# Optimization experiments

Hardware: AMD Instinct MI355X
Metric: run time of the kernel (lower is better)

## Reference

```python
import jax, jax.numpy as jnp
import numpy as np

N = 20000       # nodes
E = 640000      # random edges (self-loops appended -> E + N total)
G = 64          # graphs in batch
F_IN = 114
H1 = 3          # heads in layer 1
D2 = 128        # output_dim of layer 2
NEG = 0.2       # GATConv leaky_relu negative slope


def setup_inputs() -> dict:
    key = jax.random.key(0)
    ks = jax.random.split(key, 20)
    x = jax.random.normal(ks[0], (N, F_IN), jnp.float32)
    src = jax.random.randint(ks[1], (E,), 0, N, jnp.int32)
    dst = jax.random.randint(ks[2], (E,), 0, N, jnp.int32)
    loop = jnp.arange(N, dtype=jnp.int32)  # PyG add_self_loops=True
    edge_index = jnp.stack([jnp.concatenate([src, loop]),
                            jnp.concatenate([dst, loop])])
    batch = (jnp.arange(N) * G // N).astype(jnp.int32)  # every graph non-empty

    def lin(k, i, o):
        return jax.random.normal(k, (i, o), jnp.float32) * (1.0 / np.sqrt(i))

    return {
        "x": x, "edge_index": edge_index, "batch": batch,
        # GATConv 1: 114 -> 114 per head, 3 heads, concat
        "W1": lin(ks[3], F_IN, H1 * F_IN),
        "a_src1": jax.random.normal(ks[4], (H1, F_IN), jnp.float32) * 0.1,
        "a_dst1": jax.random.normal(ks[5], (H1, F_IN), jnp.float32) * 0.1,
        "b1": jnp.zeros((H1 * F_IN,), jnp.float32),
        # GATConv 2: 342 -> 128, 1 head
        "W2": lin(ks[6], H1 * F_IN, D2),
        "a_src2": jax.random.normal(ks[7], (1, D2), jnp.float32) * 0.1,
        "a_dst2": jax.random.normal(ks[8], (1, D2), jnp.float32) * 0.1,
        "b2": jnp.zeros((D2,), jnp.float32),
        # MLP head
        "Wg": lin(ks[9], D2, 64),  "bg": jnp.zeros((64,), jnp.float32),
        "Wf1": lin(ks[10], 64, 32), "bf1": jnp.zeros((32,), jnp.float32),
        "Wf2": lin(ks[11], 32, 16), "bf2": jnp.zeros((16,), jnp.float32),
        "Wo": lin(ks[12], 16, 1),   "bo": jnp.zeros((1,), jnp.float32),
    }


def gat_conv(x, edge_index, W, a_src, a_dst, b, heads, dim):
    """PyG GATConv (self-loops already in edge_index, eval mode)."""
    n = x.shape[0]
    h = (x @ W).reshape(n, heads, dim)             # [N,H,D]
    src, dst = edge_index[0], edge_index[1]
    alpha_s = jnp.sum(h * a_src, axis=-1)          # [N,H]
    alpha_d = jnp.sum(h * a_dst, axis=-1)          # [N,H]
    e = jax.nn.leaky_relu(alpha_s[src] + alpha_d[dst], NEG)  # [E,H]
    # segment softmax over destination nodes
    m = jax.ops.segment_max(e, dst, num_segments=n)
    ex = jnp.exp(e - m[dst])
    s = jax.ops.segment_sum(ex, dst, num_segments=n)
    alpha = ex / s[dst]                            # [E,H]
    out = jax.ops.segment_sum(h[src] * alpha[..., None], dst, num_segments=n)
    return out.reshape(n, heads * dim) + b


def reference(x, edge_index, batch, W1, a_src1, a_dst1, b1,
              W2, a_src2, a_dst2, b2, Wg, bg, Wf1, bf1, Wf2, bf2, Wo, bo):
    h = jax.nn.elu(gat_conv(x, edge_index, W1, a_src1, a_dst1, b1, H1, F_IN))
    h = jax.nn.relu(gat_conv(h, edge_index, W2, a_src2, a_dst2, b2, 1, D2))
    g = jax.ops.segment_max(h, batch, num_segments=G)   # global max pool [G,128]
    g = jax.nn.relu(g @ Wg + bg)
    g = jax.nn.relu(g @ Wf1 + bf1)
    g = jax.nn.relu(g @ Wf2 + bf2)
    return g @ Wo + bo                                  # [G,1]
```

## Files before the change

kernel.cpp:

```cpp
#include <hip/hip_runtime.h>

#define NN 20000
#define EE 660000
#define GG 64
#define FIN 114
#define H1 3
#define F1 342
#define D2 128
#define NEG 0.2f
#define H1AS 352

__device__ inline unsigned fenc(float f) {
    unsigned u = __float_as_uint(f);
    return (u & 0x80000000u) ? ~u : (u | 0x80000000u);
}
__device__ inline float fdec(unsigned u) {
    return (u & 0x80000000u) ? __uint_as_float(u & 0x7FFFFFFFu) : __uint_as_float(~u);
}
__device__ inline float lrelu(float x) { return x > 0.f ? x : NEG * x; }

__global__ void k_wa(const float* __restrict__ W1, const float* __restrict__ aS,
                     const float* __restrict__ aD, float* __restrict__ was,
                     float* __restrict__ wad) {
    int tid = blockIdx.x * 256 + threadIdx.x;
    if (tid >= 2 * FIN * H1) return;
    int which = tid >= FIN * H1;
    int i = which ? tid - FIN * H1 : tid;
    int k = i / H1, h = i % H1;
    const float* a = which ? aD : aS;
    float s = 0.f;
    for (int d = 0; d < FIN; d++) s += W1[k * F1 + h * FIN + d] * a[h * FIN + d];
    (which ? wad : was)[i] = s;
}

__global__ void k_prep1(const float* __restrict__ W1, float* __restrict__ W1P) {
    int tid = blockIdx.x * 256 + threadIdx.x;
    if (tid >= H1 * 128 * 128) return;
    int h = tid / (128 * 128);
    int rem = tid & (128 * 128 - 1);
    int k = rem >> 7, c = rem & 127;
    W1P[tid] = (c < FIN && k < FIN) ? W1[k * F1 + h * FIN + c] : 0.f;
}

__global__ __launch_bounds__(256) void k_alpha1x(const float* __restrict__ x,
                                                 const float* __restrict__ was,
                                                 const float* __restrict__ wad,
                                                 float* __restrict__ as1,
                                                 float* __restrict__ ad1) {
    int n = blockIdx.x * 4 + (threadIdx.x >> 6);
    int l = threadIdx.x & 63;
    if (n >= NN) return;
    float x0 = x[n * FIN + l];
    float x1 = (l < FIN - 64) ? x[n * FIN + 64 + l] : 0.f;
    float s[H1], d[H1];
#pragma unroll
    for (int h = 0; h < H1; h++) {
        float w0s = was[l * H1 + h], w0d = wad[l * H1 + h];
        float w1s = (l < FIN - 64) ? was[(64 + l) * H1 + h] : 0.f;
        float w1d = (l < FIN - 64) ? wad[(64 + l) * H1 + h] : 0.f;
        s[h] = x0 * w0s + x1 * w1s;
        d[h] = x0 * w0d + x1 * w1d;
    }
#pragma unroll
    for (int o = 32; o > 0; o >>= 1) {
#pragma unroll
        for (int h = 0; h < H1; h++) {
            s[h] += __shfl_down(s[h], o);
            d[h] += __shfl_down(d[h], o);
        }
    }
    if (l == 0) {
#pragma unroll
        for (int h = 0; h < H1; h++) {
            as1[n * H1 + h] = s[h];
            ad1[n * H1 + h] = d[h];
        }
    }
}

__global__ void k_count(const int* __restrict__ dst, int* __restrict__ cnt) {
    int e = blockIdx.x * 256 + threadIdx.x;
    if (e < EE) atomicAdd(&cnt[dst[e]], 1);
}

__global__ __launch_bounds__(1024) void k_scan(const int* __restrict__ cnt,
                                               int* __restrict__ off) {
    __shared__ int part[1024];
    int t = threadIdx.x;
    const int CH = 20;
    int loc[CH];
    int s = 0;
    int base = t * CH;
    for (int i = 0; i < CH; i++) {
        int idx = base + i;
        int v = (idx < NN) ? cnt[idx] : 0;
        loc[i] = s;
        s += v;
    }
    part[t] = s;
    __syncthreads();
    for (int d = 1; d < 1024; d <<= 1) {
        int v = (t >= d) ? part[t - d] : 0;
        __syncthreads();
        part[t] += v;
        __syncthreads();
    }
    int pre = (t == 0) ? 0 : part[t - 1];
    for (int i = 0; i < CH; i++) {
        int idx = base + i;
        if (idx < NN) off[idx] = pre + loc[i];
    }
    if (t == 1023) off[NN] = part[1023];
}

__global__ void k_scatter(const int* __restrict__ src, const int* __restrict__ dst,
                          const int* __restrict__ off, int* __restrict__ cur,
                          int* __restrict__ csr_src) {
    int e = blockIdx.x * 256 + threadIdx.x;
    if (e < EE) {
        int d = dst[e];
        int pos = off[d] + atomicAdd(&cur[d], 1);
        csr_src[pos] = src[e];
    }
}

__global__ __launch_bounds__(128) void k_aggx(const float* __restrict__ x,
                                              const float* __restrict__ as1,
                                              const float* __restrict__ ad1,
                                              const int* __restrict__ off,
                                              const int* __restrict__ csr_src,
                                              float* __restrict__ xaggP) {
    int n = blockIdx.x, t = threadIdx.x;
    int e0 = off[n], e1 = off[n + 1];
    float adv0 = ad1[n * H1 + 0], adv1 = ad1[n * H1 + 1], adv2 = ad1[n * H1 + 2];
    __shared__ int ssrc[64];
    __shared__ float sw[64][H1];
    __shared__ float red[64][H1];
    float acc0 = 0.f, acc1 = 0.f, acc2 = 0.f;
    float ps0 = 0.f, ps1 = 0.f, ps2 = 0.f;
    for (int base = e0; base < e1; base += 64) {
        int c = min(64, e1 - base);
        __syncthreads();
        if (t < c) {
            int s = csr_src[base + t];
            ssrc[t] = s;
            float w0 = __expf(lrelu(as1[s * H1 + 0] + adv0));
            float w1 = __expf(lrelu(as1[s * H1 + 1] + adv1));
            float w2 = __expf(lrelu(as1[s * H1 + 2] + adv2));
            sw[t][0] = w0; sw[t][1] = w1; sw[t][2] = w2;
            ps0 += w0; ps1 += w1; ps2 += w2;
        }
        __syncthreads();
        if (t < FIN) {
            for (int j = 0; j < c; j++) {
                float xv = x[ssrc[j] * FIN + t];
                acc0 += xv * sw[j][0];
                acc1 += xv * sw[j][1];
                acc2 += xv * sw[j][2];
            }
        }
    }
    __syncthreads();
    if (t < 64) { red[t][0] = ps0; red[t][1] = ps1; red[t][2] = ps2; }
    __syncthreads();
    for (int sr = 32; sr > 0; sr >>= 1) {
        if (t < sr) {
            red[t][0] += red[t + sr][0];
            red[t][1] += red[t + sr][1];
            red[t][2] += red[t + sr][2];
        }
        __syncthreads();
    }
    float i0 = 1.f / red[0][0], i1 = 1.f / red[0][1], i2 = 1.f / red[0][2];
    float v0 = (t < FIN) ? acc0 * i0 : 0.f;
    float v1 = (t < FIN) ? acc1 * i1 : 0.f;
    float v2 = (t < FIN) ? acc2 * i2 : 0.f;
    xaggP[(size_t)0 * NN * 128 + n * 128 + t] = v0;
    xaggP[(size_t)1 * NN * 128 + n * 128 + t] = v1;
    xaggP[(size_t)2 * NN * 128 + n * 128 + t] = v2;
}

__global__ __launch_bounds__(256) void k_gemm1t(const float* __restrict__ xaggP,
                                                const float* __restrict__ W1P,
                                                const float* __restrict__ b1,
                                                float* __restrict__ h1aP) {
    int h = blockIdx.y;
    int rb = blockIdx.x * 64;
    int t = threadIdx.x;
    int tr = t >> 4, tc = t & 15;
    __shared__ float As[64][36];
    __shared__ float Bs[32][132];
    const float* Ap = xaggP + (size_t)h * NN * 128;
    const float* Bp = W1P + (size_t)h * 128 * 128;
    const float4 zf4 = make_float4(0.f, 0.f, 0.f, 0.f);

    int ar0 = t >> 3, ak0 = t & 7;
    int ar1 = 32 + ar0;
    int bk[4], bn[4];
#pragma unroll
    for (int q = 0; q < 4; q++) { int idd = t + q * 256; bk[q] = idd >> 5; bn[q] = idd & 31; }

    float4 aR[2], bR[4];
    {
        int g0 = rb + ar0, g1 = rb + ar1;
        aR[0] = (g0 < NN) ? *(const float4*)(Ap + (size_t)g0 * 128 + ak0 * 4) : zf4;
        aR[1] = (g1 < NN) ? *(const float4*)(Ap + (size_t)g1 * 128 + ak0 * 4) : zf4;
#pragma unroll
        for (int q = 0; q < 4; q++)
            bR[q] = *(const float4*)(Bp + (size_t)bk[q] * 128 + bn[q] * 4);
    }
    float acc[4][8] = {};
    for (int tile = 0; tile < 4; tile++) {
        if (tile) __syncthreads();
        *(float4*)(&As[ar0][ak0 * 4]) = aR[0];
        *(float4*)(&As[ar1][ak0 * 4]) = aR[1];
#pragma unroll
        for (int q = 0; q < 4; q++) *(float4*)(&Bs[bk[q]][bn[q] * 4]) = bR[q];
        __syncthreads();
        if (tile < 3) {
            int k0 = (tile + 1) * 32;
            int g0 = rb + ar0, g1 = rb + ar1;
            aR[0] = (g0 < NN) ? *(const float4*)(Ap + (size_t)g0 * 128 + k0 + ak0 * 4) : zf4;
            aR[1] = (g1 < NN) ? *(const float4*)(Ap + (size_t)g1 * 128 + k0 + ak0 * 4) : zf4;
#pragma unroll
            for (int q = 0; q < 4; q++)
                bR[q] = *(const float4*)(Bp + (size_t)(k0 + bk[q]) * 128 + bn[q] * 4);
        }
#pragma unroll
        for (int kc = 0; kc < 32; kc += 4) {
            float a4[4][4];
#pragma unroll
            for (int r = 0; r < 4; r++)
                *(float4*)a4[r] = *(const float4*)(&As[tr * 4 + r][kc]);
#pragma unroll
            for (int kk = 0; kk < 4; kk++) {
                float4 b0 = *(const float4*)(&Bs[kc + kk][tc * 4]);
                float4 b1v = *(const float4*)(&Bs[kc + kk][64 + tc * 4]);
#pragma unroll
                for (int r = 0; r < 4; r++) {
                    float av = a4[r][kk];
                    acc[r][0] += av * b0.x;  acc[r][1] += av * b0.y;
                    acc[r][2] += av * b0.z;  acc[r][3] += av * b0.w;
                    acc[r][4] += av * b1v.x; acc[r][5] += av * b1v.y;
                    acc[r][6] += av * b1v.z; acc[r][7] += av * b1v.w;
                }
            }
        }
    }
    int hb = h * FIN;
#pragma unroll
    for (int r = 0; r < 4; r++) {
        int row = rb + tr * 4 + r;
        if (row >= NN) continue;
        float* orow = h1aP + (size_t)row * H1AS + hb;
#pragma unroll
        for (int j = 0; j < 8; j++) {
            int c = (j < 4) ? (tc * 4 + j) : (64 + tc * 4 + (j - 4));
            if (c < FIN) {
                float v = acc[r][j] + b1[hb + c];
                orow[c] = v > 0.f ? v : expm1f(v);
            } else if (h == 2 && c < 124) {
                orow[c] = 0.f;
            }
        }
    }
}

__global__ __launch_bounds__(256) void k_gemm2t(const float* __restrict__ h1aP,
                                                const float* __restrict__ W2,
                                                float* __restrict__ h2) {
    int mt = blockIdx.x >> 1, nb = (blockIdx.x & 1) * 64;
    int rb = mt * 64;
    int t = threadIdx.x;
    int tr = t >> 4, tc = t & 15;
    __shared__ float As[64][36];
    __shared__ float Bs[32][68];
    const float4 zf4 = make_float4(0.f, 0.f, 0.f, 0.f);
    int ar0 = t >> 3, ak0 = t & 7;
    int ar1 = 32 + ar0;
    int bk0 = t >> 4, bn0 = t & 15;
    int bk1 = 16 + bk0;
    float4 aR[2], bR[2];
    {
        int g0 = rb + ar0, g1 = rb + ar1;
        aR[0] = (g0 < NN) ? *(const float4*)(h1aP + (size_t)g0 * H1AS + ak0 * 4) : zf4;
        aR[1] = (g1 < NN) ? *(const float4*)(h1aP + (size_t)g1 * H1AS + ak0 * 4) : zf4;
        bR[0] = *(const float4*)(W2 + (size_t)bk0 * D2 + nb + bn0 * 4);
        bR[1] = *(const float4*)(W2 + (size_t)bk1 * D2 + nb + bn0 * 4);
    }
    float acc[4][4] = {};
    for (int tile = 0; tile < 11; tile++) {
        if (tile) __syncthreads();
        *(float4*)(&As[ar0][ak0 * 4]) = aR[0];
        *(float4*)(&As[ar1][ak0 * 4]) = aR[1];
        *(float4*)(&Bs[bk0][bn0 * 4]) = bR[0];
        *(float4*)(&Bs[bk1][bn0 * 4]) = bR[1];
        __syncthreads();
        if (tile < 10) {
            int k0 = (tile + 1) * 32;
            int g0 = rb + ar0, g1 = rb + ar1;
            aR[0] = (g0 < NN) ? *(const float4*)(h1aP + (size_t)g0 * H1AS + k0 + ak0 * 4) : zf4;
            aR[1] = (g1 < NN) ? *(const float4*)(h1aP + (size_t)g1 * H1AS + k0 + ak0 * 4) : zf4;
            bR[0] = (k0 + bk0 < F1) ? *(const float4*)(W2 + (size_t)(k0 + bk0) * D2 + nb + bn0 * 4) : zf4;
            bR[1] = (k0 + bk1 < F1) ? *(const float4*)(W2 + (size_t)(k0 + bk1) * D2 + nb + bn0 * 4) : zf4;
        }
#pragma unroll
        for (int kc = 0; kc < 32; kc += 4) {
            float a4[4][4];
#pragma unroll
            for (int r = 0; r < 4; r++)
                *(float4*)a4[r] = *(const float4*)(&As[tr * 4 + r][kc]);
#pragma unroll
            for (int kk = 0; kk < 4; kk++) {
                float4 b0 = *(const float4*)(&Bs[kc + kk][tc * 4]);
#pragma unroll
                for (int r = 0; r < 4; r++) {
                    float av = a4[r][kk];
                    acc[r][0] += av * b0.x; acc[r][1] += av * b0.y;
                    acc[r][2] += av * b0.z; acc[r][3] += av * b0.w;
                }
            }
        }
    }
#pragma unroll
    for (int r = 0; r < 4; r++) {
        int row = rb + tr * 4 + r;
        if (row < NN)
            *(float4*)(&h2[(size_t)row * D2 + nb + tc * 4]) =
                make_float4(acc[r][0], acc[r][1], acc[r][2], acc[r][3]);
    }
}

__global__ __launch_bounds__(256) void k_alpha2(const float* __restrict__ h2,
                                                const float* __restrict__ aS,
                                                const float* __restrict__ aD,
                                                float* __restrict__ as2,
                                                float* __restrict__ ad2) {
    int n = blockIdx.x * 4 + (threadIdx.x >> 6);
    int l = threadIdx.x & 63;
    if (n >= NN) return;
    float v0 = h2[(size_t)n * D2 + l], v1 = h2[(size_t)n * D2 + 64 + l];
    float ps = v0 * aS[l] + v1 * aS[64 + l];
    float pd = v0 * aD[l] + v1 * aD[64 + l];
    for (int o = 32; o > 0; o >>= 1) {
        ps += __shfl_down(ps, o);
        pd += __shfl_down(pd, o);
    }
    if (l == 0) {
        as2[n] = ps;
        ad2[n] = pd;
    }
}

__global__ __launch_bounds__(128) void k_agg2f(const float* __restrict__ h2,
                                               const float* __restrict__ as2,
                                               const float* __restrict__ ad2,
                                               const int* __restrict__ off,
                                               const int* __restrict__ csr_src,
                                               const float* __restrict__ b2,
                                               unsigned* __restrict__ poolbuf) {
    int n = blockIdx.x, t = threadIdx.x;
    int e0 = off[n], e1 = off[n + 1];
    float adv = ad2[n];
    __shared__ int ssrc[64];
    __shared__ float sw[64];
    __shared__ float red[64];
    float acc = 0.f, ps = 0.f;
    for (int base = e0; base < e1; base += 64) {
        int c = min(64, e1 - base);
        __syncthreads();
        if (t < c) {
            int s = csr_src[base + t];
            ssrc[t] = s;
            float w = __expf(lrelu(as2[s] + adv));
            sw[t] = w;
            ps += w;
        }
        __syncthreads();
        for (int j = 0; j < c; j++) acc += h2[(size_t)ssrc[j] * D2 + t] * sw[j];
    }
    __syncthreads();
    if (t < 64) red[t] = ps;
    __syncthreads();
    for (int sr = 32; sr > 0; sr >>= 1) {
        if (t < sr) red[t] += red[t + sr];
        __syncthreads();
    }
    float v = fmaxf(acc / red[0] + b2[t], 0.f);
    int g = (int)(((long long)n * GG) / NN);
    atomicMax(&poolbuf[g * D2 + t], fenc(v));
}

__global__ __launch_bounds__(128) void k_mlp(const unsigned* __restrict__ poolbuf,
                                             const float* __restrict__ Wg,
                                             const float* __restrict__ bg,
                                             const float* __restrict__ Wf1,
                                             const float* __restrict__ bf1,
                                             const float* __restrict__ Wf2,
                                             const float* __restrict__ bf2,
                                             const float* __restrict__ Wo,
                                             const float* __restrict__ bo,
                                             float* __restrict__ out) {
    int g = blockIdx.x;
    int t = threadIdx.x;
    __shared__ float pool[D2];
    __shared__ float a1[64];
    __shared__ float a2[32];
    __shared__ float a3[16];
    pool[t] = fdec(poolbuf[g * D2 + t]);
    __syncthreads();
    if (t < 64) {
        float acc = bg[t];
        for (int k = 0; k < D2; k++) acc += pool[k] * Wg[k * 64 + t];
        a1[t] = fmaxf(acc, 0.f);
    }
    __syncthreads();
    if (t < 32) {
        float acc = bf1[t];
        for (int k = 0; k < 64; k++) acc += a1[k] * Wf1[k * 32 + t];
        a2[t] = fmaxf(acc, 0.f);
    }
    __syncthreads();
    if (t < 16) {
        float acc = bf2[t];
        for (int k = 0; k < 32; k++) acc += a2[k] * Wf2[k * 16 + t];
        a3[t] = fmaxf(acc, 0.f);
    }
    __syncthreads();
    if (t == 0) {
        float acc = bo[0];
        for (int k = 0; k < 16; k++) acc += a3[k] * Wo[k];
        out[g] = acc;
    }
}

extern "C" void kernel_launch(void* const* d_in, const int* in_sizes, int n_in,
                              void* d_out, int out_size, void* d_ws, size_t ws_size,
                              hipStream_t stream) {
    const float* x = (const float*)d_in[0];
    const int* ei = (const int*)d_in[1];
    const float* W1 = (const float*)d_in[3];
    const float* aS1 = (const float*)d_in[4];
    const float* aD1 = (const float*)d_in[5];
    const float* b1 = (const float*)d_in[6];
    const float* W2 = (const float*)d_in[7];
    const float* aS2 = (const float*)d_in[8];
    const float* aD2 = (const float*)d_in[9];
    const float* b2 = (const float*)d_in[10];
    const float* Wg = (const float*)d_in[11];
    const float* bg = (const float*)d_in[12];
    const float* Wf1 = (const float*)d_in[13];
    const float* bf1 = (const float*)d_in[14];
    const float* Wf2 = (const float*)d_in[15];
    const float* bf2 = (const float*)d_in[16];
    const float* Wo = (const float*)d_in[17];
    const float* bo = (const float*)d_in[18];
    float* out = (float*)d_out;

    const int* src = ei;
    const int* dst = ei + EE;

    char* ws = (char*)d_ws;
    size_t o = 0;
    auto alloc = [&](size_t bytes) -> char* {
        char* p = ws + o;
        o += (bytes + 255) & ~(size_t)255;
        return p;
    };
    float* was = (float*)alloc((size_t)FIN * H1 * 4);
    float* wad = (float*)alloc((size_t)FIN * H1 * 4);
    float* W1P = (float*)alloc((size_t)H1 * 128 * 128 * 4);
    float* as1 = (float*)alloc((size_t)NN * H1 * 4);
    float* ad1 = (float*)alloc((size_t)NN * H1 * 4);
    int* cnt = (int*)alloc((size_t)NN * 4);
    int* off = (int*)alloc((size_t)(NN + 1) * 4);
    int* cur = (int*)alloc((size_t)NN * 4);
    int* csr_src = (int*)alloc((size_t)EE * 4);
    float* xaggP = (float*)alloc((size_t)H1 * NN * 128 * 4);
    float* h1aP = (float*)alloc((size_t)NN * H1AS * 4);
    float* h2 = (float*)alloc((size_t)NN * D2 * 4);
    float* as2 = (float*)alloc((size_t)NN * 4);
    float* ad2 = (float*)alloc((size_t)NN * 4);
    unsigned* poolbuf = (unsigned*)alloc((size_t)GG * D2 * 4);
    (void)ws_size;

    hipMemsetAsync(cnt, 0, (size_t)NN * 4, stream);
    hipMemsetAsync(cur, 0, (size_t)NN * 4, stream);
    hipMemsetAsync(poolbuf, 0, (size_t)GG * D2 * 4, stream);

    const int EB = (EE + 255) / 256;

    k_wa<<<(2 * FIN * H1 + 255) / 256, 256, 0, stream>>>(W1, aS1, aD1, was, wad);
    k_prep1<<<(H1 * 128 * 128 + 255) / 256, 256, 0, stream>>>(W1, W1P);
    k_alpha1x<<<(NN + 3) / 4, 256, 0, stream>>>(x, was, wad, as1, ad1);
    k_count<<<EB, 256, 0, stream>>>(dst, cnt);
    k_scan<<<1, 1024, 0, stream>>>(cnt, off);
    k_scatter<<<EB, 256, 0, stream>>>(src, dst, off, cur, csr_src);
    k_aggx<<<NN, 128, 0, stream>>>(x, as1, ad1, off, csr_src, xaggP);
    k_gemm1t<<<dim3((NN + 63) / 64, H1), 256, 0, stream>>>(xaggP, W1P, b1, h1aP);
    k_gemm2t<<<((NN + 63) / 64) * 2, 256, 0, stream>>>(h1aP, W2, h2);
    k_alpha2<<<(NN + 3) / 4, 256, 0, stream>>>(h2, aS2, aD2, as2, ad2);
    k_agg2f<<<NN, 128, 0, stream>>>(h2, as2, ad2, off, csr_src, b2, poolbuf);
    k_mlp<<<GG, 128, 0, stream>>>(poolbuf, Wg, bg, Wf1, bf1, Wf2, bf2, Wo, bo, out);
}
```

Measured before the change: 319.4 us.

## Replace FP32 SIMT GEMMs with split-bf16 MFMA GEMMs

Both dense GEMMs (layer-1 per-head projection and layer-2 projection) now run on matrix cores using bf16 MFMA 16x16x32. Each FP32 operand is split into hi and lo bf16 halves, and three products (hi*hi, hi*lo, lo*hi) are summed to keep close to FP32 accuracy. Weights are pre-transposed and split, and the aggregation and GEMM1 epilogues store split bf16 pairs instead of floats, which also changes the intermediate layout to a head-major padded format. The new kernels load operands straight from global memory without LDS staging, which may cost bandwidth. The 3x MFMA count and the split overhead are traded for higher matrix-core throughput.

```diff
diff --git a/kernel.cpp b/kernel.cpp
--- a/kernel.cpp
+++ b/kernel.cpp
@@ -8,7 +8,10 @@
 #define F1 342
 #define D2 128
 #define NEG 0.2f
-#define H1AS 352
+
+typedef __attribute__((ext_vector_type(8))) short short8v;
+typedef __attribute__((ext_vector_type(4))) float f32x4;
+typedef unsigned short ushort_t;
 
 __device__ inline unsigned fenc(float f) {
     unsigned u = __float_as_uint(f);
@@ -18,6 +21,16 @@
     return (u & 0x80000000u) ? __uint_as_float(u & 0x7FFFFFFFu) : __uint_as_float(~u);
 }
 __device__ inline float lrelu(float x) { return x > 0.f ? x : NEG * x; }
+
+__device__ inline void split2(float x, ushort_t& hi, ushort_t& lo) {
+    unsigned u = __float_as_uint(x);
+    unsigned uh = u & 0xFFFF0000u;
+    hi = (ushort_t)(uh >> 16);
+    float r = x - __uint_as_float(uh);
+    unsigned v = __float_as_uint(r);
+    unsigned vh = (v + 0x7FFFu + ((v >> 16) & 1u)) & 0xFFFF0000u;
+    lo = (ushort_t)(vh >> 16);
+}
 
 __global__ void k_wa(const float* __restrict__ W1, const float* __restrict__ aS,
                      const float* __restrict__ aD, float* __restrict__ was,
@@ -33,13 +46,32 @@
     (which ? wad : was)[i] = s;
 }
 
-__global__ void k_prep1(const float* __restrict__ W1, float* __restrict__ W1P) {
+__global__ void k_prep1m(const float* __restrict__ W1, ushort_t* __restrict__ W1Th,
+                         ushort_t* __restrict__ W1Tl) {
     int tid = blockIdx.x * 256 + threadIdx.x;
     if (tid >= H1 * 128 * 128) return;
     int h = tid / (128 * 128);
     int rem = tid & (128 * 128 - 1);
-    int k = rem >> 7, c = rem & 127;
-    W1P[tid] = (c < FIN && k < FIN) ? W1[k * F1 + h * FIN + c] : 0.f;
+    int c = rem >> 7, k = rem & 127;
+    float v = (c < FIN && k < FIN) ? W1[k * F1 + h * FIN + c] : 0.f;
+    ushort_t hi, lo;
+    split2(v, hi, lo);
+    W1Th[tid] = hi;
+    W1Tl[tid] = lo;
+}
+
+__global__ void k_prep2m(const float* __restrict__ W2, ushort_t* __restrict__ W2Th,
+                         ushort_t* __restrict__ W2Tl) {
+    int tid = blockIdx.x * 256 + threadIdx.x;
+    if (tid >= 128 * 384) return;
+    int c = tid / 384;
+    int hk = tid - c * 384;
+    int h = hk >> 7, k = hk & 127;
+    float v = (k < FIN) ? W2[(h * FIN + k) * D2 + c] : 0.f;
+    ushort_t hi, lo;
+    split2(v, hi, lo);
+    W2Th[tid] = hi;
+    W2Tl[tid] = lo;
 }
 
 __global__ __launch_bounds__(256) void k_alpha1x(const float* __restrict__ x,
@@ -129,7 +161,8 @@
                                               const float* __restrict__ ad1,
                                               const int* __restrict__ off,
                                               const int* __restrict__ csr_src,
-                                              float* __restrict__ xaggP) {
+                                              ushort_t* __restrict__ xgh,
+                                              ushort_t* __restrict__ xgl) {
     int n = blockIdx.x, t = threadIdx.x;
     int e0 = off[n], e1 = off[n + 1];
     float adv0 = ad1[n * H1 + 0], adv1 = ad1[n * H1 + 1], adv2 = ad1[n * H1 + 2];
@@ -175,159 +208,107 @@
     float v0 = (t < FIN) ? acc0 * i0 : 0.f;
     float v1 = (t < FIN) ? acc1 * i1 : 0.f;
     float v2 = (t < FIN) ? acc2 * i2 : 0.f;
-    xaggP[(size_t)0 * NN * 128 + n * 128 + t] = v0;
-    xaggP[(size_t)1 * NN * 128 + n * 128 + t] = v1;
-    xaggP[(size_t)2 * NN * 128 + n * 128 + t] = v2;
-}
-
-__global__ __launch_bounds__(256) void k_gemm1t(const float* __restrict__ xaggP,
-                                                const float* __restrict__ W1P,
+    ushort_t hi, lo;
+    split2(v0, hi, lo);
+    xgh[(size_t)0 * NN * 128 + n * 128 + t] = hi;
+    xgl[(size_t)0 * NN * 128 + n * 128 + t] = lo;
+    split2(v1, hi, lo);
+    xgh[(size_t)1 * NN * 128 + n * 128 + t] = hi;
+    xgl[(size_t)1 * NN * 128 + n * 128 + t] = lo;
+    split2(v2, hi, lo);
+    xgh[(size_t)2 * NN * 128 + n * 128 + t] = hi;
+    xgl[(size_t)2 * NN * 128 + n * 128 + t] = lo;
+}
+
+__global__ __launch_bounds__(256) void k_gemm1m(const ushort_t* __restrict__ xgh,
+                                                const ushort_t* __restrict__ xgl,
+                                                const ushort_t* __restrict__ W1Th,
+                                                const ushort_t* __restrict__ W1Tl,
                                                 const float* __restrict__ b1,
-                                                float* __restrict__ h1aP) {
+                                                ushort_t* __restrict__ h1hi,
+                                                ushort_t* __restrict__ h1lo) {
     int h = blockIdx.y;
     int rb = blockIdx.x * 64;
-    int t = threadIdx.x;
-    int tr = t >> 4, tc = t & 15;
-    __shared__ float As[64][36];
-    __shared__ float Bs[32][132];
-    const float* Ap = xaggP + (size_t)h * NN * 128;
-    const float* Bp = W1P + (size_t)h * 128 * 128;
-    const float4 zf4 = make_float4(0.f, 0.f, 0.f, 0.f);
-
-    int ar0 = t >> 3, ak0 = t & 7;
-    int ar1 = 32 + ar0;
-    int bk[4], bn[4];
-#pragma unroll
-    for (int q = 0; q < 4; q++) { int idd = t + q * 256; bk[q] = idd >> 5; bn[q] = idd & 31; }
-
-    float4 aR[2], bR[4];
-    {
-        int g0 = rb + ar0, g1 = rb + ar1;
-        aR[0] = (g0 < NN) ? *(const float4*)(Ap + (size_t)g0 * 128 + ak0 * 4) : zf4;
-        aR[1] = (g1 < NN) ? *(const float4*)(Ap + (size_t)g1 * 128 + ak0 * 4) : zf4;
-#pragma unroll
-        for (int q = 0; q < 4; q++)
-            bR[q] = *(const float4*)(Bp + (size_t)bk[q] * 128 + bn[q] * 4);
-    }
-    float acc[4][8] = {};
-    for (int tile = 0; tile < 4; tile++) {
-        if (tile) __syncthreads();
-        *(float4*)(&As[ar0][ak0 * 4]) = aR[0];
-        *(float4*)(&As[ar1][ak0 * 4]) = aR[1];
-#pragma unroll
-        for (int q = 0; q < 4; q++) *(float4*)(&Bs[bk[q]][bn[q] * 4]) = bR[q];
-        __syncthreads();
-        if (tile < 3) {
-            int k0 = (tile + 1) * 32;
-            int g0 = rb + ar0, g1 = rb + ar1;
-            aR[0] = (g0 < NN) ? *(const float4*)(Ap + (size_t)g0 * 128 + k0 + ak0 * 4) : zf4;
-            aR[1] = (g1 < NN) ? *(const float4*)(Ap + (size_t)g1 * 128 + k0 + ak0 * 4) : zf4;
-#pragma unroll
-            for (int q = 0; q < 4; q++)
-                bR[q] = *(const float4*)(Bp + (size_t)(k0 + bk[q]) * 128 + bn[q] * 4);
-        }
-#pragma unroll
-        for (int kc = 0; kc < 32; kc += 4) {
-            float a4[4][4];
-#pragma unroll
-            for (int r = 0; r < 4; r++)
-                *(float4*)a4[r] = *(const float4*)(&As[tr * 4 + r][kc]);
-#pragma unroll
-            for (int kk = 0; kk < 4; kk++) {
-                float4 b0 = *(const float4*)(&Bs[kc + kk][tc * 4]);
-                float4 b1v = *(const float4*)(&Bs[kc + kk][64 + tc * 4]);
-#pragma unroll
-                for (int r = 0; r < 4; r++) {
-                    float av = a4[r][kk];
-                    acc[r][0] += av * b0.x;  acc[r][1] += av * b0.y;
-                    acc[r][2] += av * b0.z;  acc[r][3] += av * b0.w;
-                    acc[r][4] += av * b1v.x; acc[r][5] += av * b1v.y;
-                    acc[r][6] += av * b1v.z; acc[r][7] += av * b1v.w;
-                }
-            }
-        }
-    }
-    int hb = h * FIN;
-#pragma unroll
-    for (int r = 0; r < 4; r++) {
-        int row = rb + tr * 4 + r;
-        if (row >= NN) continue;
-        float* orow = h1aP + (size_t)row * H1AS + hb;
+    int w = threadIdx.x >> 6, l = threadIdx.x & 63;
+    int m = l & 15, g = l >> 4;
+    int row = rb + w * 16 + m;
+    bool rok = (row < NN);
+    const size_t abase = ((size_t)h * NN + (size_t)(rok ? row : 0)) * 128;
+    const short8v z8 = {0, 0, 0, 0, 0, 0, 0, 0};
+    f32x4 acc[8];
+#pragma unroll
+    for (int j = 0; j < 8; j++) acc[j] = (f32x4){0.f, 0.f, 0.f, 0.f};
+    for (int k0 = 0; k0 < 128; k0 += 32) {
+        short8v ah = rok ? *(const short8v*)(xgh + abase + k0 + g * 8) : z8;
+        short8v al = rok ? *(const short8v*)(xgl + abase + k0 + g * 8) : z8;
 #pragma unroll
         for (int j = 0; j < 8; j++) {
-            int c = (j < 4) ? (tc * 4 + j) : (64 + tc * 4 + (j - 4));
-            if (c < FIN) {
-                float v = acc[r][j] + b1[hb + c];
-                orow[c] = v > 0.f ? v : expm1f(v);
-            } else if (h == 2 && c < 124) {
-                orow[c] = 0.f;
-            }
-        }
-    }
-}
-
-__global__ __launch_bounds__(256) void k_gemm2t(const float* __restrict__ h1aP,
-                                                const float* __restrict__ W2,
+            int c = j * 16 + m;
+            size_t bo = ((size_t)h * 128 + c) * 128 + k0 + g * 8;
+            short8v bh = *(const short8v*)(W1Th + bo);
+            short8v bl = *(const short8v*)(W1Tl + bo);
+            acc[j] = __builtin_amdgcn_mfma_f32_16x16x32_bf16(ah, bh, acc[j], 0, 0, 0);
+            acc[j] = __builtin_amdgcn_mfma_f32_16x16x32_bf16(ah, bl, acc[j], 0, 0, 0);
+            acc[j] = __builtin_amdgcn_mfma_f32_16x16x32_bf16(al, bh, acc[j], 0, 0, 0);
+        }
+    }
+#pragma unroll
+    for (int j = 0; j < 8; j++) {
+        int c = j * 16 + m;
+        float bv = (c < FIN) ? b1[h * FIN + c] : 0.f;
+#pragma unroll
+        for (int r = 0; r < 4; r++) {
+            int orow = rb + w * 16 + g * 4 + r;
+            if (orow >= NN) continue;
+            float v = acc[j][r] + bv;
+            v = v > 0.f ? v : expm1f(v);
+            ushort_t hi = 0, lo = 0;
+            if (c < FIN) split2(v, hi, lo);
+            size_t oo = ((size_t)h * NN + orow) * 128 + c;
+            h1hi[oo] = hi;
+            h1lo[oo] = lo;
+        }
+    }
+}
+
+__global__ __launch_bounds__(256) void k_gemm2m(const ushort_t* __restrict__ h1hi,
+                                                const ushort_t* __restrict__ h1lo,
+                                                const ushort_t* __restrict__ W2Th,
+                                                const ushort_t* __restrict__ W2Tl,
                                                 float* __restrict__ h2) {
-    int mt = blockIdx.x >> 1, nb = (blockIdx.x & 1) * 64;
-    int rb = mt * 64;
-    int t = threadIdx.x;
-    int tr = t >> 4, tc = t & 15;
-    __shared__ float As[64][36];
-    __shared__ float Bs[32][68];
-    const float4 zf4 = make_float4(0.f, 0.f, 0.f, 0.f);
-    int ar0 = t >> 3, ak0 = t & 7;
-    int ar1 = 32 + ar0;
-    int bk0 = t >> 4, bn0 = t & 15;
-    int bk1 = 16 + bk0;
-    float4 aR[2], bR[2];
-    {
-        int g0 = rb + ar0, g1 = rb + ar1;
-        aR[0] = (g0 < NN) ? *(const float4*)(h1aP + (size_t)g0 * H1AS + ak0 * 4) : zf4;
-        aR[1] = (g1 < NN) ? *(const float4*)(h1aP + (size_t)g1 * H1AS + ak0 * 4) : zf4;
-        bR[0] = *(const float4*)(W2 + (size_t)bk0 * D2 + nb + bn0 * 4);
-        bR[1] = *(const float4*)(W2 + (size_t)bk1 * D2 + nb + bn0 * 4);
-    }
-    float acc[4][4] = {};
-    for (int tile = 0; tile < 11; tile++) {
-        if (tile) __syncthreads();
-        *(float4*)(&As[ar0][ak0 * 4]) = aR[0];
-        *(float4*)(&As[ar1][ak0 * 4]) = aR[1];
-        *(float4*)(&Bs[bk0][bn0 * 4]) = bR[0];
-        *(float4*)(&Bs[bk1][bn0 * 4]) = bR[1];
-        __syncthreads();
-        if (tile < 10) {
-            int k0 = (tile + 1) * 32;
-            int g0 = rb + ar0, g1 = rb + ar1;
-            aR[0] = (g0 < NN) ? *(const float4*)(h1aP + (size_t)g0 * H1AS + k0 + ak0 * 4) : zf4;
-            aR[1] = (g1 < NN) ? *(const float4*)(h1aP + (size_t)g1 * H1AS + k0 + ak0 * 4) : zf4;
-            bR[0] = (k0 + bk0 < F1) ? *(const float4*)(W2 + (size_t)(k0 + bk0) * D2 + nb + bn0 * 4) : zf4;
-            bR[1] = (k0 + bk1 < F1) ? *(const float4*)(W2 + (size_t)(k0 + bk1) * D2 + nb + bn0 * 4) : zf4;
-        }
-#pragma unroll
-        for (int kc = 0; kc < 32; kc += 4) {
-            float a4[4][4];
-#pragma unroll
-            for (int r = 0; r < 4; r++)
-                *(float4*)a4[r] = *(const float4*)(&As[tr * 4 + r][kc]);
-#pragma unroll
-            for (int kk = 0; kk < 4; kk++) {
-                float4 b0 = *(const float4*)(&Bs[kc + kk][tc * 4]);
-#pragma unroll
-                for (int r = 0; r < 4; r++) {
-                    float av = a4[r][kk];
-                    acc[r][0] += av * b0.x; acc[r][1] += av * b0.y;
-                    acc[r][2] += av * b0.z; acc[r][3] += av * b0.w;
-                }
-            }
-        }
-    }
-#pragma unroll
-    for (int r = 0; r < 4; r++) {
-        int row = rb + tr * 4 + r;
-        if (row < NN)
-            *(float4*)(&h2[(size_t)row * D2 + nb + tc * 4]) =
-                make_float4(acc[r][0], acc[r][1], acc[r][2], acc[r][3]);
+    int rb = blockIdx.x * 64;
+    int w = threadIdx.x >> 6, l = threadIdx.x & 63;
+    int m = l & 15, g = l >> 4;
+    int row = rb + w * 16 + m;
+    bool rok = (row < NN);
+    const short8v z8 = {0, 0, 0, 0, 0, 0, 0, 0};
+    f32x4 acc[8];
+#pragma unroll
+    for (int j = 0; j < 8; j++) acc[j] = (f32x4){0.f, 0.f, 0.f, 0.f};
+    for (int k0 = 0; k0 < 384; k0 += 32) {
+        int hh = k0 >> 7, kc = (k0 & 127) + g * 8;
+        size_t ao = ((size_t)hh * NN + (size_t)(rok ? row : 0)) * 128 + kc;
+        short8v ah = rok ? *(const short8v*)(h1hi + ao) : z8;
+        short8v al = rok ? *(const short8v*)(h1lo + ao) : z8;
+#pragma unroll
+        for (int j = 0; j < 8; j++) {
+            int c = j * 16 + m;
+            size_t bo = (size_t)c * 384 + k0 + g * 8;
+            short8v bh = *(const short8v*)(W2Th + bo);
+            short8v bl = *(const short8v*)(W2Tl + bo);
+            acc[j] = __builtin_amdgcn_mfma_f32_16x16x32_bf16(ah, bh, acc[j], 0, 0, 0);
+            acc[j] = __builtin_amdgcn_mfma_f32_16x16x32_bf16(ah, bl, acc[j], 0, 0, 0);
+            acc[j] = __builtin_amdgcn_mfma_f32_16x16x32_bf16(al, bh, acc[j], 0, 0, 0);
+        }
+    }
+#pragma unroll
+    for (int j = 0; j < 8; j++) {
+        int c = j * 16 + m;
+#pragma unroll
+        for (int r = 0; r < 4; r++) {
+            int orow = rb + w * 16 + g * 4 + r;
+            if (orow < NN) h2[(size_t)orow * D2 + c] = acc[j][r];
+        }
     }
 }
 
@@ -469,15 +450,20 @@
     };
     float* was = (float*)alloc((size_t)FIN * H1 * 4);
     float* wad = (float*)alloc((size_t)FIN * H1 * 4);
-    float* W1P = (float*)alloc((size_t)H1 * 128 * 128 * 4);
+    ushort_t* W1Th = (ushort_t*)alloc((size_t)H1 * 128 * 128 * 2);
+    ushort_t* W1Tl = (ushort_t*)alloc((size_t)H1 * 128 * 128 * 2);
+    ushort_t* W2Th = (ushort_t*)alloc((size_t)128 * 384 * 2);
+    ushort_t* W2Tl = (ushort_t*)alloc((size_t)128 * 384 * 2);
     float* as1 = (float*)alloc((size_t)NN * H1 * 4);
     float* ad1 = (float*)alloc((size_t)NN * H1 * 4);
     int* cnt = (int*)alloc((size_t)NN * 4);
     int* off = (int*)alloc((size_t)(NN + 1) * 4);
     int* cur = (int*)alloc((size_t)NN * 4);
     int* csr_src = (int*)alloc((size_t)EE * 4);
-    float* xaggP = (float*)alloc((size_t)H1 * NN * 128 * 4);
-    float* h1aP = (float*)alloc((size_t)NN * H1AS * 4);
+    ushort_t* xgh = (ushort_t*)alloc((size_t)H1 * NN * 128 * 2);
+    ushort_t* xgl = (ushort_t*)alloc((size_t)H1 * NN * 128 * 2);
+    ushort_t* h1hi = (ushort_t*)alloc((size_t)H1 * NN * 128 * 2);
+    ushort_t* h1lo = (ushort_t*)alloc((size_t)H1 * NN * 128 * 2);
     float* h2 = (float*)alloc((size_t)NN * D2 * 4);
     float* as2 = (float*)alloc((size_t)NN * 4);
     float* ad2 = (float*)alloc((size_t)NN * 4);
@@ -491,14 +477,15 @@
     const int EB = (EE + 255) / 256;
 
     k_wa<<<(2 * FIN * H1 + 255) / 256, 256, 0, stream>>>(W1, aS1, aD1, was, wad);
-    k_prep1<<<(H1 * 128 * 128 + 255) / 256, 256, 0, stream>>>(W1, W1P);
+    k_prep1m<<<(H1 * 128 * 128 + 255) / 256, 256, 0, stream>>>(W1, W1Th, W1Tl);
+    k_prep2m<<<(128 * 384 + 255) / 256, 256, 0, stream>>>(W2, W2Th, W2Tl);
     k_alpha1x<<<(NN + 3) / 4, 256, 0, stream>>>(x, was, wad, as1, ad1);
     k_count<<<EB, 256, 0, stream>>>(dst, cnt);
     k_scan<<<1, 1024, 0, stream>>>(cnt, off);
     k_scatter<<<EB, 256, 0, stream>>>(src, dst, off, cur, csr_src);
-    k_aggx<<<NN, 128, 0, stream>>>(x, as1, ad1, off, csr_src, xaggP);
-    k_gemm1t<<<dim3((NN + 63) / 64, H1), 256, 0, stream>>>(xaggP, W1P, b1, h1aP);
-    k_gemm2t<<<((NN + 63) / 64) * 2, 256, 0, stream>>>(h1aP, W2, h2);
+    k_aggx<<<NN, 128, 0, stream>>>(x, as1, ad1, off, csr_src, xgh, xgl);
+    k_gemm1m<<<dim3((NN + 63) / 64, H1), 256, 0, stream>>>(xgh, xgl, W1Th, W1Tl, b1, h1hi, h1lo);
+    k_gemm2m<<<(NN + 63) / 64, 256, 0, stream>>>(h1hi, h1lo, W2Th, W2Tl, h2);
     k_alpha2<<<(NN + 3) / 4, 256, 0, stream>>>(h2, aS2, aD2, as2, ad2);
     k_agg2f<<<NN, 128, 0, stream>>>(h2, as2, ad2, off, csr_src, b2, poolbuf);
     k_mlp<<<GG, 128, 0, stream>>>(poolbuf, Wg, bg, Wf1, bf1, Wf2, bf2, Wo, bo, out);
```

After: 328.6 us. 1.03x slower.
